# Optimization experiments

Hardware: AMD Instinct MI355X
Metric: run time of the kernel (lower is better)

The kernel has to match this reference:

```python
import jax, jax.numpy as jnp
import numpy as np

N = 50000      # nodes
E = 800000     # edges (before self-loops)
F_IN = 128     # num_features
HID = 32       # hidden channels per head (conv1)
HEADS = 4      # conv1 heads
C = 40         # classes (conv2 out channels)
OUT_HEADS = 1  # conv2 heads
NEG_SLOPE = 0.2


def setup_inputs() -> dict:
    key = jax.random.key(0)
    ks = jax.random.split(key, 10)
    x = jax.random.normal(ks[0], (N, F_IN), jnp.float32)
    edge_index = jax.random.randint(ks[1], (2, E), 0, N, jnp.int32)
    s1 = 1.0 / np.sqrt(F_IN).astype(np.float32)
    s1h = 1.0 / np.sqrt(HID).astype(np.float32)
    s2 = 1.0 / np.sqrt(HEADS * HID).astype(np.float32)
    s2c = 1.0 / np.sqrt(C).astype(np.float32)
    W1 = jax.random.normal(ks[2], (F_IN, HEADS * HID), jnp.float32) * s1
    att_src1 = jax.random.normal(ks[3], (HEADS, HID), jnp.float32) * s1h
    att_dst1 = jax.random.normal(ks[4], (HEADS, HID), jnp.float32) * s1h
    bias1 = jnp.zeros((HEADS * HID,), jnp.float32)
    W2 = jax.random.normal(ks[5], (HEADS * HID, OUT_HEADS * C), jnp.float32) * s2
    att_src2 = jax.random.normal(ks[6], (OUT_HEADS, C), jnp.float32) * s2c
    att_dst2 = jax.random.normal(ks[7], (OUT_HEADS, C), jnp.float32) * s2c
    bias2 = jnp.zeros((C,), jnp.float32)
    return {"x": x, "edge_index": edge_index,
            "W1": W1, "att_src1": att_src1, "att_dst1": att_dst1, "bias1": bias1,
            "W2": W2, "att_src2": att_src2, "att_dst2": att_dst2, "bias2": bias2}


def gat_layer(h_in, src, dst, W, a_src, a_dst, bias, heads, out_ch, concat):
    """PyG GATConv (v1) in inference mode (no dropout on attention)."""
    n = h_in.shape[0]
    h = (h_in @ W).reshape(n, heads, out_ch)              # [N,H,F]
    e_src = jnp.einsum('nhf,hf->nh', h, a_src)            # [N,H]
    e_dst = jnp.einsum('nhf,hf->nh', h, a_dst)            # [N,H]
    alpha = jax.nn.leaky_relu(e_src[src] + e_dst[dst], NEG_SLOPE)  # [E,H]
    # segment softmax over destination-node neighborhoods
    amax = jax.ops.segment_max(alpha, dst, num_segments=n)
    amax = jnp.where(jnp.isfinite(amax), amax, 0.0)
    ex = jnp.exp(alpha - amax[dst])
    denom = jax.ops.segment_sum(ex, dst, num_segments=n)
    coef = ex / (denom[dst] + 1e-16)                      # [E,H]
    # scatter-aggregate weighted source messages
    out = jax.ops.segment_sum(h[src] * coef[:, :, None], dst, num_segments=n)  # [N,H,F]
    out = out.reshape(n, heads * out_ch) if concat else out.mean(axis=1)
    return out + bias


def reference(x, edge_index, W1, att_src1, att_dst1, bias1, W2, att_src2, att_dst2, bias2):
    n = x.shape[0]
    loop = jnp.arange(n, dtype=edge_index.dtype)          # GATConv adds self-loops
    src = jnp.concatenate([edge_index[0], loop])
    dst = jnp.concatenate([edge_index[1], loop])
    h = jax.nn.elu(gat_layer(x, src, dst, W1, att_src1, att_dst1, bias1, HEADS, HID, True))
    out = gat_layer(h, src, dst, W2, att_src2, att_dst2, bias2, OUT_HEADS, C, False)
    return (jax.nn.log_softmax(out, axis=1), jax.nn.softmax(out, axis=1))
```

## Files before the change

kernel.cpp:

```cpp
#include <hip/hip_runtime.h>
#include <hip/hip_bf16.h>

#define F1   128
#define H1   4
#define C2   40
#define NEG  0.2f
#define DS   96

typedef __hip_bfloat16 bf16;
typedef float f32x2 __attribute__((ext_vector_type(2)));
typedef short s16x8 __attribute__((ext_vector_type(8)));
typedef float f32x4 __attribute__((ext_vector_type(4)));

__device__ __forceinline__ float ldf(const void* p, size_t i, int isbf) {
    return isbf ? __bfloat162float(((const bf16*)p)[i]) : ((const float*)p)[i];
}
__device__ __forceinline__ float lrelu(float a) { return a > 0.f ? a : NEG * a; }

__device__ __forceinline__ unsigned short f2bfb(float f, float& back) {
    unsigned u = __float_as_uint(f);
    unsigned r = u + 0x7FFFu + ((u >> 16) & 1u);
    unsigned short h = (unsigned short)(r >> 16);
    back = __uint_as_float((unsigned)h << 16);
    return h;
}

__device__ __forceinline__ void up2(unsigned g, float& lo, float& hi) {
    lo = __uint_as_float(g << 16);
    hi = __uint_as_float(g & 0xffff0000u);
}
__device__ __forceinline__ f32x2 up2v(unsigned g) {
    f32x2 r;
    r.x = __uint_as_float(g << 16);
    r.y = __uint_as_float(g & 0xffff0000u);
    return r;
}

__global__ void k_prep(const unsigned short* __restrict__ x, int* __restrict__ deg,
                       int N, int* __restrict__ flag) {
    int i = blockIdx.x * 256 + threadIdx.x;
    if (i < N) deg[i] = 0;
    if (blockIdx.x == 0) {
        __shared__ int sh[256];
        int cnt = 0;
        for (int k = threadIdx.x; k < 8192; k += 256)
            if (((x[k] >> 7) & 0xFF) >= 160) cnt++;
        sh[threadIdx.x] = cnt;
        __syncthreads();
        for (int s = 128; s > 0; s >>= 1) {
            if (threadIdx.x < s) sh[threadIdx.x] += sh[threadIdx.x + s];
            __syncthreads();
        }
        if (threadIdx.x == 0) flag[0] = (sh[0] < 100) ? 1 : 0;
    }
}

__global__ void k_wprep(const void* __restrict__ W1, const int* __restrict__ flag,
                        unsigned short* __restrict__ w1t_hi,
                        unsigned short* __restrict__ w1t_lo) {
    int idx = blockIdx.x * 256 + threadIdx.x;
    int k = idx >> 7, c = idx & 127;
    const int isbf = flag[0];
    float v = ldf(W1, idx, isbf);
    float back;
    unsigned short hi = f2bfb(v, back);
    float d2;
    unsigned short lo = f2bfb(v - back, d2);
    w1t_hi[c * 128 + k] = hi;
    w1t_lo[c * 128 + k] = isbf ? (unsigned short)0 : lo;
}

__global__ void __launch_bounds__(256) k_gemm1(
        const void* __restrict__ x, const unsigned short* __restrict__ w1t_hi,
        const unsigned short* __restrict__ w1t_lo,
        const void* __restrict__ as1, const void* __restrict__ ad1,
        const int* __restrict__ flag, const int* __restrict__ ei,
        int E, int ET, int* __restrict__ deg, int* __restrict__ ebuf2,
        bf16* __restrict__ h1b, float* __restrict__ es1, float* __restrict__ ed1,
        int N) {
    int per = (ET + gridDim.x - 1) / gridDim.x;
    int he0 = blockIdx.x * per;
    int he1 = he0 + per; if (he1 > ET) he1 = ET;
    for (int e = he0 + threadIdx.x; e < he1; e += 256) {
        int s, d;
        if (e < E) { s = ei[e]; d = ei[E + e]; }
        else       { s = e - E; d = e - E; }
        int pos = atomicAdd(&deg[d], 1);
        if (pos < DS) ebuf2[d * DS + pos] = s;
    }
    const int isbf = flag[0];
    int t = threadIdx.x, wv = t >> 6, l = t & 63;
    int r0 = (wv & 1) * 16, c0 = (wv >> 1) * 64;
    int lr = l & 15, q = l >> 4;
    int n0 = blockIdx.x * 32;
    int rowa = n0 + r0 + lr; if (rowa >= N) rowa = N - 1;

    const bf16*  xb = (const bf16*)x;
    const float* xf = (const float*)x;
    f32x4 acc[4] = {};

#pragma unroll
    for (int ks = 0; ks < 4; ks++) {
        int kb = ks * 32 + q * 8;
        s16x8 ahi, alo;
        if (isbf) {
            ahi = *(const s16x8*)&xb[(size_t)rowa * 128 + kb];
        } else {
            const float* xr = xf + (size_t)rowa * 128 + kb;
            float4 v0 = *(const float4*)xr;
            float4 v1 = *(const float4*)(xr + 4);
            float vv[8] = {v0.x, v0.y, v0.z, v0.w, v1.x, v1.y, v1.z, v1.w};
#pragma unroll
            for (int j = 0; j < 8; j++) {
                float back;
                unsigned short hb = f2bfb(vv[j], back);
                float d2;
                unsigned short lb = f2bfb(vv[j] - back, d2);
                ahi[j] = (short)hb;
                alo[j] = (short)lb;
            }
        }
#pragma unroll
        for (int f = 0; f < 4; f++) {
            int col = c0 + f * 16 + lr;
            s16x8 bh = *(const s16x8*)&w1t_hi[(size_t)col * 128 + kb];
            acc[f] = __builtin_amdgcn_mfma_f32_16x16x32_bf16(ahi, bh, acc[f], 0, 0, 0);
            if (!isbf) {
                s16x8 bl = *(const s16x8*)&w1t_lo[(size_t)col * 128 + kb];
                acc[f] = __builtin_amdgcn_mfma_f32_16x16x32_bf16(alo, bh, acc[f], 0, 0, 0);
                acc[f] = __builtin_amdgcn_mfma_f32_16x16x32_bf16(ahi, bl, acc[f], 0, 0, 0);
            }
        }
    }

    float asv[4], adv[4];
#pragma unroll
    for (int f = 0; f < 4; f++) {
        asv[f] = ldf(as1, c0 + f * 16 + lr, isbf);
        adv[f] = ldf(ad1, c0 + f * 16 + lr, isbf);
    }
    float ps0[4], ps1[4], pd0[4], pd1[4];
#pragma unroll
    for (int r = 0; r < 4; r++) {
        int rw = n0 + r0 + q * 4 + r;
        ps0[r] = acc[0][r] * asv[0] + acc[1][r] * asv[1];
        ps1[r] = acc[2][r] * asv[2] + acc[3][r] * asv[3];
        pd0[r] = acc[0][r] * adv[0] + acc[1][r] * adv[1];
        pd1[r] = acc[2][r] * adv[2] + acc[3][r] * adv[3];
        if (rw < N) {
#pragma unroll
            for (int f = 0; f < 4; f++)
                h1b[(size_t)rw * 128 + c0 + f * 16 + lr] = __float2bfloat16(acc[f][r]);
        }
    }
#pragma unroll
    for (int off = 1; off < 16; off <<= 1) {
#pragma unroll
        for (int r = 0; r < 4; r++) {
            ps0[r] += __shfl_xor(ps0[r], off, 64);
            ps1[r] += __shfl_xor(ps1[r], off, 64);
            pd0[r] += __shfl_xor(pd0[r], off, 64);
            pd1[r] += __shfl_xor(pd1[r], off, 64);
        }
    }
    if (lr == 0) {
        int h0 = c0 >> 5;
#pragma unroll
        for (int r = 0; r < 4; r++) {
            int rw = n0 + r0 + q * 4 + r;
            if (rw < N) {
                es1[rw * H1 + h0]     = ps0[r];
                es1[rw * H1 + h0 + 1] = ps1[r];
                ed1[rw * H1 + h0]     = pd0[r];
                ed1[rw * H1 + h0 + 1] = pd1[r];
            }
        }
    }
}

__global__ void __launch_bounds__(256) k_l1(
        const int* __restrict__ deg, const int* __restrict__ ebuf2,
        const float* __restrict__ es1, const float* __restrict__ ed1,
        const uint4* __restrict__ h1p4, const void* __restrict__ b1,
        const void* __restrict__ W2, const void* __restrict__ as2,
        const void* __restrict__ ad2, const int* __restrict__ flag,
        bf16* __restrict__ h2b, float* __restrict__ es2, float* __restrict__ ed2,
        int N) {
    int w = threadIdx.x >> 6, l = threadIdx.x & 63;
    int d = blockIdx.x * 4 + w; if (d >= N) d = N - 1;
    int cnt = deg[d]; if (cnt > DS) cnt = DS;
    int start = d * DS;

    __shared__ int   s_sh[4][DS];
    __shared__ float ev_sh[4][4][DS + 4];
    __shared__ float hs[4][F1];

    float4 edv = *(const float4*)&ed1[(size_t)d * 4];
    float t0 = 0.f, t1 = 0.f, t2 = 0.f, t3 = 0.f;
    if (l < cnt) {
        int s = ebuf2[start + l];
        s_sh[w][l] = s;
        float4 es4 = *(const float4*)&es1[(size_t)s * 4];
        float v0 = __expf(lrelu(es4.x + edv.x));
        float v1 = __expf(lrelu(es4.y + edv.y));
        float v2 = __expf(lrelu(es4.z + edv.z));
        float v3 = __expf(lrelu(es4.w + edv.w));
        ev_sh[w][0][l] = v0; ev_sh[w][1][l] = v1;
        ev_sh[w][2][l] = v2; ev_sh[w][3][l] = v3;
        t0 = v0; t1 = v1; t2 = v2; t3 = v3;
    }
    if (cnt > 64) {
        int l2 = 64 + l;
        if (l2 < cnt) {
            int s = ebuf2[start + l2];
            s_sh[w][l2] = s;
            float4 es4 = *(const float4*)&es1[(size_t)s * 4];
            float v0 = __expf(lrelu(es4.x + edv.x));
            float v1 = __expf(lrelu(es4.y + edv.y));
            float v2 = __expf(lrelu(es4.z + edv.z));
            float v3 = __expf(lrelu(es4.w + edv.w));
            ev_sh[w][0][l2] = v0; ev_sh[w][1][l2] = v1;
            ev_sh[w][2][l2] = v2; ev_sh[w][3][l2] = v3;
            t0 += v0; t1 += v1; t2 += v2; t3 += v3;
        }
    }
#pragma unroll
    for (int off = 32; off > 0; off >>= 1) {
        t0 += __shfl_xor(t0, off, 64);
        t1 += __shfl_xor(t1, off, 64);
        t2 += __shfl_xor(t2, off, 64);
        t3 += __shfl_xor(t3, off, 64);
    }
    __syncthreads();

    int q = l >> 4, c16 = l & 15, h = c16 >> 2;
    f32x2 acc[4] = {{0.f, 0.f}, {0.f, 0.f}, {0.f, 0.f}, {0.f, 0.f}};
    for (int i = 0; i < cnt; i += 16) {
#pragma unroll
        for (int u = 0; u < 4; u++) {
            int e = i + q + 4 * u;
            int ec = min(e, cnt - 1);
            float evh = (e < cnt) ? ev_sh[w][h][ec] : 0.f;
            int s = s_sh[w][ec];
            uint4 g = h1p4[(size_t)s * 16 + c16];
            f32x2 ev2 = {evh, evh};
            acc[0] += ev2 * up2v(g.x);
            acc[1] += ev2 * up2v(g.y);
            acc[2] += ev2 * up2v(g.z);
            acc[3] += ev2 * up2v(g.w);
        }
    }

#pragma unroll
    for (int off = 16; off <= 32; off <<= 1) {
#pragma unroll
        for (int jj = 0; jj < 4; jj++) {
            acc[jj].x += __shfl_xor(acc[jj].x, off, 64);
            acc[jj].y += __shfl_xor(acc[jj].y, off, 64);
        }
    }

    const int isbf = flag[0];
    float dsum = (h == 0) ? t0 : (h == 1) ? t1 : (h == 2) ? t2 : t3;
    if (q == 0) {
        float inv = 1.f / (dsum + 1e-16f);
#pragma unroll
        for (int j = 0; j < 8; j++) {
            int col = c16 * 8 + j;
            float av = (j & 1) ? acc[j >> 1].y : acc[j >> 1].x;
            float v = av * inv + ldf(b1, col, isbf);
            hs[w][col] = v > 0.f ? v : (__expf(v) - 1.f);
        }
    }
    __syncthreads();
    float a2 = 0.f;
    if (l < C2) {
        if (isbf) {
            const bf16* W = (const bf16*)W2;
#pragma unroll
            for (int k4 = 0; k4 < 32; k4++) {
                float4 hv = *(const float4*)&hs[w][k4 * 4];
                int kb = k4 * 4;
                a2 = fmaf(hv.x, __bfloat162float(W[(size_t)kb * C2 + l]), a2);
                a2 = fmaf(hv.y, __bfloat162float(W[(size_t)(kb + 1) * C2 + l]), a2);
                a2 = fmaf(hv.z, __bfloat162float(W[(size_t)(kb + 2) * C2 + l]), a2);
                a2 = fmaf(hv.w, __bfloat162float(W[(size_t)(kb + 3) * C2 + l]), a2);
            }
        } else {
            const float* W = (const float*)W2;
#pragma unroll
            for (int k4 = 0; k4 < 32; k4++) {
                float4 hv = *(const float4*)&hs[w][k4 * 4];
                int kb = k4 * 4;
                a2 = fmaf(hv.x, W[(size_t)kb * C2 + l], a2);
                a2 = fmaf(hv.y, W[(size_t)(kb + 1) * C2 + l], a2);
                a2 = fmaf(hv.z, W[(size_t)(kb + 2) * C2 + l], a2);
                a2 = fmaf(hv.w, W[(size_t)(kb + 3) * C2 + l], a2);
            }
        }
        h2b[(size_t)d * C2 + l] = __float2bfloat16(a2);
    }
    float ps = (l < C2) ? a2 * ldf(as2, l, isbf) : 0.f;
    float pd = (l < C2) ? a2 * ldf(ad2, l, isbf) : 0.f;
#pragma unroll
    for (int off = 32; off > 0; off >>= 1) {
        ps += __shfl_xor(ps, off, 64);
        pd += __shfl_xor(pd, off, 64);
    }
    if (l == 0) { es2[d] = ps; ed2[d] = pd; }
}

__global__ void __launch_bounds__(256) k_l2(
        const int* __restrict__ deg, const int* __restrict__ ebuf2,
        const float* __restrict__ es2, const float* __restrict__ ed2,
        const unsigned* __restrict__ h2p, const void* __restrict__ b2,
        const int* __restrict__ flag, void* __restrict__ out, int N) {
    int w = threadIdx.x >> 6, l = threadIdx.x & 63;
    int d = blockIdx.x * 4 + w; if (d >= N) d = N - 1;
    int cnt = deg[d]; if (cnt > DS) cnt = DS;
    int start = d * DS;
    float edd = ed2[d];

    __shared__ int   s_sh2[4][DS];
    __shared__ float x_sh[4][DS];

    float xv = 0.f;
    if (l < cnt) {
        int s = ebuf2[start + l];
        s_sh2[w][l] = s;
        xv = __expf(lrelu(es2[s] + edd));
        x_sh[w][l] = xv;
    }
    float dsum = xv;
    if (cnt > 64) {
        int l2 = 64 + l;
        if (l2 < cnt) {
            int s = ebuf2[start + l2];
            s_sh2[w][l2] = s;
            float x2 = __expf(lrelu(es2[s] + edd));
            x_sh[w][l2] = x2;
            dsum += x2;
        }
    }
#pragma unroll
    for (int off = 32; off > 0; off >>= 1) dsum += __shfl_xor(dsum, off, 64);
    __syncthreads();

    int half = l >> 5, j = l & 31;
    float acc0 = 0.f, acc1 = 0.f;
    if (j < 20) {
        for (int i = 0; i < cnt; i += 16) {
#pragma unroll
            for (int u = 0; u < 8; u++) {
                int e = i + half * 8 + u;
                int ec = min(e, cnt - 1);
                float x = (e < cnt) ? x_sh[w][ec] : 0.f;
                int s = s_sh2[w][ec];
                unsigned g = h2p[(size_t)s * 20 + j];
                float lo, hi; up2(g, lo, hi);
                acc0 = fmaf(x, lo, acc0);
                acc1 = fmaf(x, hi, acc1);
            }
        }
        acc0 += __shfl_xor(acc0, 32, 64);
        acc1 += __shfl_xor(acc1, 32, 64);
    }

    const int isbf = flag[0];
    float inv = 1.f / (dsum + 1e-16f);
    float v0 = -1e30f, v1 = -1e30f;
    if (l < 20) {
        v0 = acc0 * inv + ldf(b2, 2 * l, isbf);
        v1 = acc1 * inv + ldf(b2, 2 * l + 1, isbf);
    }
    float m = fmaxf(v0, v1);
#pragma unroll
    for (int off = 16; off > 0; off >>= 1) m = fmaxf(m, __shfl_xor(m, off, 32));
    float sv = (l < 20) ? __expf(v0 - m) + __expf(v1 - m) : 0.f;
#pragma unroll
    for (int off = 16; off > 0; off >>= 1) sv += __shfl_xor(sv, off, 32);
    float lse = m + __logf(sv);
    if (l < 20) {
        float ls0 = v0 - lse, ls1 = v1 - lse;
        size_t base = (size_t)d * C2 + 2 * l, halfo = (size_t)N * C2;
        if (isbf) {
            bf16* o = (bf16*)out;
            o[base] = __float2bfloat16(ls0);
            o[base + 1] = __float2bfloat16(ls1);
            o[halfo + base] = __float2bfloat16(__expf(ls0));
            o[halfo + base + 1] = __float2bfloat16(__expf(ls1));
        } else {
            float* o = (float*)out;
            o[base] = ls0;
            o[base + 1] = ls1;
            o[halfo + base] = __expf(ls0);
            o[halfo + base + 1] = __expf(ls1);
        }
    }
}

extern "C" void kernel_launch(void* const* d_in, const int* in_sizes, int n_in,
                              void* d_out, int out_size, void* d_ws, size_t ws_size,
                              hipStream_t stream) {
    const int N  = in_sizes[0] / F1;
    const int E  = in_sizes[1] / 2;
    const int ET = E + N;
    const int NB = (N + 255) / 256;

    const void* x   = d_in[0];
    const int*  ei  = (const int*)d_in[1];
    const void* W1  = d_in[2];
    const void* as1 = d_in[3];
    const void* ad1 = d_in[4];
    const void* b1  = d_in[5];
    const void* W2  = d_in[6];
    const void* as2 = d_in[7];
    const void* ad2 = d_in[8];
    const void* b2  = d_in[9];

    float* ws = (float*)d_ws;
    auto al4 = [](size_t v) { return (v + 3) & ~(size_t)3; };
    size_t o = 0;
    bf16*  h1b  = (bf16*)(ws + o); o = al4(o + (size_t)64 * N);
    float* es1  = ws + o; o = al4(o + (size_t)H1 * N);
    float* ed1  = ws + o; o = al4(o + (size_t)H1 * N);
    bf16*  h2b  = (bf16*)(ws + o); o = al4(o + (size_t)20 * N);
    float* es2  = ws + o; o = al4(o + N);
    float* ed2  = ws + o; o = al4(o + N);
    int*   deg  = (int*)(ws + o); o = al4(o + N);
    int*   flag = (int*)(ws + o); o = al4(o + 4);
    int*   ebuf2 = (int*)(ws + o); o = al4(o + (size_t)DS * N);
    unsigned short* w1t_hi = (unsigned short*)(ws + o); o = al4(o + 8192);
    unsigned short* w1t_lo = (unsigned short*)(ws + o); o = al4(o + 8192);

    k_prep<<<NB, 256, 0, stream>>>((const unsigned short*)x, deg, N, flag);
    k_wprep<<<64, 256, 0, stream>>>(W1, flag, w1t_hi, w1t_lo);
    k_gemm1<<<(N + 31) / 32, 256, 0, stream>>>(x, w1t_hi, w1t_lo, as1, ad1, flag,
                                               ei, E, ET, deg, ebuf2, h1b, es1, ed1, N);
    k_l1<<<(N + 3) / 4, 256, 0, stream>>>(deg, ebuf2, es1, ed1, (const uint4*)h1b,
                                          b1, W2, as2, ad2, flag, h2b, es2, ed2, N);
    k_l2<<<(N + 3) / 4, 256, 0, stream>>>(deg, ebuf2, es2, ed2, (const unsigned*)h2b,
                                          b2, flag, d_out, N);
}
```

Measured before the change: 324.8 us.

## Split edge scatter into its own kernel and pad shared hidden buffer

Moves the edge bucketing (atomic degree count plus source scatter) out of the GEMM1 kernel into a separate one-edge-per-thread kernel, so the GEMM no longer waits on atomics before its matrix work. It also pads the per-wave hidden vector in shared memory by one float every 8 and replaces the float4 reads in the layer-2 projection loop with scalar reads, to change the LDS bank access pattern. The cost is one extra kernel launch, and the edge scatter no longer overlaps with GEMM1.

```diff
diff --git a/kernel.cpp b/kernel.cpp
--- a/kernel.cpp
+++ b/kernel.cpp
@@ -70,24 +70,25 @@
     w1t_lo[c * 128 + k] = isbf ? (unsigned short)0 : lo;
 }
 
+__global__ void __launch_bounds__(256) k_scat(const int* __restrict__ ei, int E, int ET,
+                                              int* __restrict__ deg,
+                                              int* __restrict__ ebuf2) {
+    int e = blockIdx.x * 256 + threadIdx.x;
+    if (e >= ET) return;
+    int s, d;
+    if (e < E) { s = ei[e]; d = ei[E + e]; }
+    else       { s = e - E; d = e - E; }
+    int pos = atomicAdd(&deg[d], 1);
+    if (pos < DS) ebuf2[d * DS + pos] = s;
+}
+
 __global__ void __launch_bounds__(256) k_gemm1(
         const void* __restrict__ x, const unsigned short* __restrict__ w1t_hi,
         const unsigned short* __restrict__ w1t_lo,
         const void* __restrict__ as1, const void* __restrict__ ad1,
-        const int* __restrict__ flag, const int* __restrict__ ei,
-        int E, int ET, int* __restrict__ deg, int* __restrict__ ebuf2,
+        const int* __restrict__ flag,
         bf16* __restrict__ h1b, float* __restrict__ es1, float* __restrict__ ed1,
         int N) {
-    int per = (ET + gridDim.x - 1) / gridDim.x;
-    int he0 = blockIdx.x * per;
-    int he1 = he0 + per; if (he1 > ET) he1 = ET;
-    for (int e = he0 + threadIdx.x; e < he1; e += 256) {
-        int s, d;
-        if (e < E) { s = ei[e]; d = ei[E + e]; }
-        else       { s = e - E; d = e - E; }
-        int pos = atomicAdd(&deg[d], 1);
-        if (pos < DS) ebuf2[d * DS + pos] = s;
-    }
     const int isbf = flag[0];
     int t = threadIdx.x, wv = t >> 6, l = t & 63;
     int r0 = (wv & 1) * 16, c0 = (wv >> 1) * 64;
@@ -193,7 +194,7 @@
 
     __shared__ int   s_sh[4][DS];
     __shared__ float ev_sh[4][4][DS + 4];
-    __shared__ float hs[4][F1];
+    __shared__ float hs[4][144];
 
     float4 edv = *(const float4*)&ed1[(size_t)d * 4];
     float t0 = 0.f, t1 = 0.f, t2 = 0.f, t3 = 0.f;
@@ -269,7 +270,7 @@
             int col = c16 * 8 + j;
             float av = (j & 1) ? acc[j >> 1].y : acc[j >> 1].x;
             float v = av * inv + ldf(b1, col, isbf);
-            hs[w][col] = v > 0.f ? v : (__expf(v) - 1.f);
+            hs[w][col + (col >> 3)] = v > 0.f ? v : (__expf(v) - 1.f);
         }
     }
     __syncthreads();
@@ -277,26 +278,14 @@
     if (l < C2) {
         if (isbf) {
             const bf16* W = (const bf16*)W2;
-#pragma unroll
-            for (int k4 = 0; k4 < 32; k4++) {
-                float4 hv = *(const float4*)&hs[w][k4 * 4];
-                int kb = k4 * 4;
-                a2 = fmaf(hv.x, __bfloat162float(W[(size_t)kb * C2 + l]), a2);
-                a2 = fmaf(hv.y, __bfloat162float(W[(size_t)(kb + 1) * C2 + l]), a2);
-                a2 = fmaf(hv.z, __bfloat162float(W[(size_t)(kb + 2) * C2 + l]), a2);
-                a2 = fmaf(hv.w, __bfloat162float(W[(size_t)(kb + 3) * C2 + l]), a2);
-            }
+#pragma unroll 8
+            for (int k = 0; k < F1; k++)
+                a2 = fmaf(hs[w][k + (k >> 3)], __bfloat162float(W[(size_t)k * C2 + l]), a2);
         } else {
             const float* W = (const float*)W2;
-#pragma unroll
-            for (int k4 = 0; k4 < 32; k4++) {
-                float4 hv = *(const float4*)&hs[w][k4 * 4];
-                int kb = k4 * 4;
-                a2 = fmaf(hv.x, W[(size_t)kb * C2 + l], a2);
-                a2 = fmaf(hv.y, W[(size_t)(kb + 1) * C2 + l], a2);
-                a2 = fmaf(hv.z, W[(size_t)(kb + 2) * C2 + l], a2);
-                a2 = fmaf(hv.w, W[(size_t)(kb + 3) * C2 + l], a2);
-            }
+#pragma unroll 8
+            for (int k = 0; k < F1; k++)
+                a2 = fmaf(hs[w][k + (k >> 3)], W[(size_t)k * C2 + l], a2);
         }
         h2b[(size_t)d * C2 + l] = __float2bfloat16(a2);
     }
@@ -435,8 +424,9 @@
 
     k_prep<<<NB, 256, 0, stream>>>((const unsigned short*)x, deg, N, flag);
     k_wprep<<<64, 256, 0, stream>>>(W1, flag, w1t_hi, w1t_lo);
+    k_scat<<<(ET + 255) / 256, 256, 0, stream>>>(ei, E, ET, deg, ebuf2);
     k_gemm1<<<(N + 31) / 32, 256, 0, stream>>>(x, w1t_hi, w1t_lo, as1, ad1, flag,
-                                               ei, E, ET, deg, ebuf2, h1b, es1, ed1, N);
+                                               h1b, es1, ed1, N);
     k_l1<<<(N + 3) / 4, 256, 0, stream>>>(deg, ebuf2, es1, ed1, (const uint4*)h1b,
                                           b1, W2, as2, ad2, flag, h2b, es2, ed2, N);
     k_l2<<<(N + 3) / 4, 256, 0, stream>>>(deg, ebuf2, es2, ed2, (const unsigned*)h2b,
```

Measured after the change: 313.2 us. 1.04x faster.
